# Performance work log

Measured on AMD Instinct MI355X. Metric: run time of the kernel, lower is better.

Reference implementation:

```python
import jax, jax.numpy as jnp
import numpy as np

N_NODES = 50000
N_EDGES = 600000
D = 128
N_LAYERS = 4  # 2 base + 2 resnet layers
N_GRAPHS = 64
NEG_SLOPE = 0.01  # F.leaky_relu default


def setup_inputs() -> dict:
    key = jax.random.key(0)
    k1, k2, k3, k4, k5 = jax.random.split(key, 5)
    x = jax.random.normal(k1, (N_NODES, D), dtype=jnp.float32)
    edge_index = jax.random.randint(k2, (2, N_EDGES), 0, N_NODES, dtype=jnp.int64)
    batch = jnp.sort(jax.random.randint(k3, (N_NODES,), 0, N_GRAPHS, dtype=jnp.int64))
    Wl = jax.random.normal(k4, (N_LAYERS, D, D), dtype=jnp.float32) * 0.05
    bl = jnp.zeros((N_LAYERS, D), dtype=jnp.float32)
    Wr = jax.random.normal(k5, (N_LAYERS, D, D), dtype=jnp.float32) * 0.05
    return {"x": x, "edge_index": edge_index, "batch": batch,
            "Wl": Wl, "bl": bl, "Wr": Wr}


def _mean_aggregate(x, src, dst, n_nodes):
    # mean over incoming neighbors; isolated nodes get 0 (PyG scatter-mean semantics)
    s = jax.ops.segment_sum(x[src], dst, num_segments=n_nodes)  # [N, D]
    cnt = jax.ops.segment_sum(jnp.ones((src.shape[0],), x.dtype), dst,
                              num_segments=n_nodes)
    return s / jnp.maximum(cnt, 1.0)[:, None]


def reference(x, edge_index, batch, Wl, bl, Wr):
    src, dst = edge_index[0], edge_index[1]
    n = x.shape[0]
    for i in range(N_LAYERS):
        agg = _mean_aggregate(x, src, dst, n)                      # [N, D]
        # SAGEConv: lin_l(agg) + lin_r(x); lin_l has bias, lin_r does not
        x_new = agg @ Wl[i].T + bl[i] + x @ Wr[i].T
        x_new = jnp.where(x_new >= 0, x_new, NEG_SLOPE * x_new)    # leaky_relu
        x = x_new if i < 2 else x + x_new                          # residual after first 2
    # global mean pool per graph
    pooled = jax.ops.segment_sum(x, batch, num_segments=N_GRAPHS)  # [G, D]
    counts = jax.ops.segment_sum(jnp.ones((n,), x.dtype), batch,
                                 num_segments=N_GRAPHS)
    return pooled / jnp.maximum(counts, 1.0)[:, None]
```

## Files before the change

kernel.cpp:

```cpp
#include <hip/hip_runtime.h>

#define N_NODES 50000
#define N_EDGES 600000
#define DIM 128
#define N_LAYERS 4
#define N_GRAPHS 64
#define NEG_SLOPE 0.01f
#define NB_SCAN ((N_NODES + 255) / 256)
#define RS 264

typedef __attribute__((ext_vector_type(8))) short short8;
typedef __attribute__((ext_vector_type(16))) float floatx16;

__device__ __forceinline__ unsigned short f2bf(float f) {
    union { float f; unsigned u; } c; c.f = f;
    unsigned u = c.u;
    unsigned r = (u + 0x7FFFu + ((u >> 16) & 1u)) >> 16;
    return (unsigned short)r;
}
__device__ __forceinline__ float bfraw2f(unsigned short b) {
    union { unsigned u; float f; } c; c.u = ((unsigned)b) << 16;
    return c.f;
}
__device__ __forceinline__ float bflo(unsigned u) {
    union { unsigned u; float f; } c; c.u = u << 16; return c.f;
}
__device__ __forceinline__ float bfhi(unsigned u) {
    union { unsigned u; float f; } c; c.u = u & 0xFFFF0000u; return c.f;
}


__global__ void zero_ints(int* p, int n) {
    int i = blockIdx.x * blockDim.x + threadIdx.x;
    if (i < n) p[i] = 0;
}

__global__ void convert_x(const float4* __restrict__ x, uint4* __restrict__ xb) {
    int i = blockIdx.x * blockDim.x + threadIdx.x;
    if (i >= N_NODES * DIM / 8) return;
    float4 a = x[i * 2], b = x[i * 2 + 1];
    uint4 o;
    o.x = ((unsigned)f2bf(a.y) << 16) | f2bf(a.x);
    o.y = ((unsigned)f2bf(a.w) << 16) | f2bf(a.z);
    o.z = ((unsigned)f2bf(b.y) << 16) | f2bf(b.x);
    o.w = ((unsigned)f2bf(b.w) << 16) | f2bf(b.z);
    xb[i] = o;
}

__global__ void pack_w(const float* __restrict__ Wl, const float* __restrict__ Wr,
                       ushort* __restrict__ wpk) {
    int s = blockIdx.x >> 2, t = blockIdx.x & 3;
    int m = blockIdx.y, layer = blockIdx.z;
    int l = threadIdx.x;
    const float* W = ((m == 0) ? Wl : Wr) + (size_t)layer * DIM * DIM;
    int n = t * 32 + (l & 31);
    int kb = s * 16 + (l >> 5) * 8;
    size_t off = ((((size_t)(layer * 2 + m) * 8 + s) * 4 + t) * 64 + l) * 8;
    for (int j = 0; j < 8; j++)
        wpk[off + j] = f2bf(W[n * DIM + kb + j]);
}

__global__ void count_deg(const int* __restrict__ dst, int* deg) {
    int e = blockIdx.x * blockDim.x + threadIdx.x;
    if (e < N_EDGES) atomicAdd(&deg[dst[e]], 1);
}

__global__ void scan_pass1(const int* __restrict__ deg, int* __restrict__ bsum) {
    int i = blockIdx.x * 256 + threadIdx.x;
    int v = (i < N_NODES) ? deg[i] : 0;
    for (int off = 32; off > 0; off >>= 1) v += __shfl_down(v, off, 64);
    __shared__ int ws[4];
    int lane = threadIdx.x & 63, w = threadIdx.x >> 6;
    if (lane == 0) ws[w] = v;
    __syncthreads();
    if (threadIdx.x == 0) bsum[blockIdx.x] = ws[0] + ws[1] + ws[2] + ws[3];
}

__global__ void scan_pass2(int* __restrict__ bsum) {
    __shared__ int sm[256];
    int t = threadIdx.x;
    int v = (t < NB_SCAN) ? bsum[t] : 0;
    sm[t] = v;
    __syncthreads();
    for (int off = 1; off < 256; off <<= 1) {
        int u = (t >= off) ? sm[t - off] : 0;
        __syncthreads();
        sm[t] += u;
        __syncthreads();
    }
    if (t < NB_SCAN) bsum[t] = sm[t] - v;
}

__global__ void scan_pass3(const int* __restrict__ deg, const int* __restrict__ bsum,
                           int* __restrict__ rp) {
    int i = blockIdx.x * 256 + threadIdx.x;
    int v = (i < N_NODES) ? deg[i] : 0;
    int lane = threadIdx.x & 63, w = threadIdx.x >> 6;
    int s = v;
    for (int off = 1; off < 64; off <<= 1) {
        int t = __shfl_up(s, off, 64);
        if (lane >= off) s += t;
    }
    __shared__ int ws[4];
    if (lane == 63) ws[w] = s;
    __syncthreads();
    int wo = 0;
    for (int k = 0; k < 4; k++) wo += (k < w) ? ws[k] : 0;
    int incl = s + wo + bsum[blockIdx.x];
    if (i < N_NODES) rp[i + 1] = incl;
    if (i == 0) rp[0] = 0;
}

__global__ void fill_csr(const int* __restrict__ src, const int* __restrict__ dst,
                         const int* __restrict__ rp, int* __restrict__ fill,
                         int* __restrict__ csr) {
    int e = blockIdx.x * blockDim.x + threadIdx.x;
    if (e >= N_EDGES) return;
    int d = dst[e];
    int pos = atomicAdd(&fill[d], 1);
    csr[rp[d] + pos] = src[e];
}

__global__ void graph_start(const int* __restrict__ batch, int* __restrict__ gstart) {
    int i = blockIdx.x * blockDim.x + threadIdx.x;
    if (i >= N_NODES) return;
    int b = batch[i];
    if (i == 0) {
        for (int g = 0; g <= b; g++) gstart[g] = 0;
    } else {
        int p = batch[i - 1];
        for (int g = p + 1; g <= b; g++) gstart[g] = i;
    }
    if (i == N_NODES - 1) {
        for (int g = b + 1; g <= N_GRAPHS; g++) gstart[g] = N_NODES;
    }
}

__global__ __launch_bounds__(256) void agg_mean_bf16(const uint4* __restrict__ xb4,
                                                     const int* __restrict__ rp,
                                                     const int* __restrict__ csr,
                                                     uint4* __restrict__ agg4) {
    int node = blockIdx.x * 16 + (threadIdx.x >> 4);
    int ln = threadIdx.x & 15;
    if (node >= N_NODES) return;
    int s = rp[node], e = rp[node + 1];
    float a0 = 0.f, a1 = 0.f, a2 = 0.f, a3 = 0.f, a4 = 0.f, a5 = 0.f, a6 = 0.f, a7 = 0.f;
    int i = s;
    for (; i + 2 <= e; i += 2) {
        int n0 = csr[i], n1 = csr[i + 1];
        uint4 v0 = xb4[n0 * 16 + ln];
        uint4 v1 = xb4[n1 * 16 + ln];
        a0 += bflo(v0.x) + bflo(v1.x); a1 += bfhi(v0.x) + bfhi(v1.x);
        a2 += bflo(v0.y) + bflo(v1.y); a3 += bfhi(v0.y) + bfhi(v1.y);
        a4 += bflo(v0.z) + bflo(v1.z); a5 += bfhi(v0.z) + bfhi(v1.z);
        a6 += bflo(v0.w) + bflo(v1.w); a7 += bfhi(v0.w) + bfhi(v1.w);
    }
    if (i < e) {
        uint4 v = xb4[csr[i] * 16 + ln];
        a0 += bflo(v.x); a1 += bfhi(v.x);
        a2 += bflo(v.y); a3 += bfhi(v.y);
        a4 += bflo(v.z); a5 += bfhi(v.z);
        a6 += bflo(v.w); a7 += bfhi(v.w);
    }
    float inv = 1.0f / (float)max(e - s, 1);
    uint4 o;
    o.x = ((unsigned)f2bf(a1 * inv) << 16) | f2bf(a0 * inv);
    o.y = ((unsigned)f2bf(a3 * inv) << 16) | f2bf(a2 * inv);
    o.z = ((unsigned)f2bf(a5 * inv) << 16) | f2bf(a4 * inv);
    o.w = ((unsigned)f2bf(a7 * inv) << 16) | f2bf(a6 * inv);
    agg4[node * 16 + ln] = o;
}

__global__ __launch_bounds__(256) void fused_layer_mfma(const ushort* __restrict__ agg,
                                                        const ushort* __restrict__ xin,
                                                        ushort* __restrict__ xout,
                                                        const ushort* __restrict__ wpk,
                                                        const float* __restrict__ bias,
                                                        int residual) {
    __shared__ ushort sA[128 * RS];
    int t = threadIdx.x;
    int node0 = blockIdx.x * 128;

    const uint4* aggv = (const uint4*)(agg + (size_t)node0 * DIM);
    const uint4* xv   = (const uint4*)(xin + (size_t)node0 * DIM);
    for (int i = t; i < 128 * 32; i += 256) {
        int r = i >> 5, c = i & 31;
        uint4 val = make_uint4(0u, 0u, 0u, 0u);
        if (node0 + r < N_NODES)
            val = (c < 16) ? aggv[r * 16 + c] : xv[r * 16 + (c - 16)];
        *(uint4*)&sA[r * RS + c * 8] = val;
    }
    __syncthreads();

    int wv = t >> 6, l = t & 63;
    int m0 = wv * 32;
    const ushort* arow = &sA[(m0 + (l & 31)) * RS];
    int khalf = (l >> 5) * 8;

    floatx16 acc0, acc1, acc2, acc3;
    for (int ii = 0; ii < 16; ii++) acc0[ii] = acc1[ii] = acc2[ii] = acc3[ii] = 0.f;

    const ushort* wl8 = wpk + (size_t)l * 8;
#pragma unroll
    for (int s2 = 0; s2 < 16; s2++) {
        int m = s2 >> 3, s = s2 & 7;
        short8 a = *(const short8*)(arow + m * 128 + s * 16 + khalf);
        size_t fb = (size_t)((m * 8 + s) * 4) * 512;
        short8 b0 = *(const short8*)(wl8 + fb);
        short8 b1 = *(const short8*)(wl8 + fb + 512);
        short8 b2 = *(const short8*)(wl8 + fb + 1024);
        short8 b3 = *(const short8*)(wl8 + fb + 1536);
        acc0 = __builtin_amdgcn_mfma_f32_32x32x16_bf16(a, b0, acc0, 0, 0, 0);
        acc1 = __builtin_amdgcn_mfma_f32_32x32x16_bf16(a, b1, acc1, 0, 0, 0);
        acc2 = __builtin_amdgcn_mfma_f32_32x32x16_bf16(a, b2, acc2, 0, 0, 0);
        acc3 = __builtin_amdgcn_mfma_f32_32x32x16_bf16(a, b3, acc3, 0, 0, 0);
    }

    int col = l & 31;
    int rbase = 4 * (l >> 5);
    floatx16 accs[4] = {acc0, acc1, acc2, acc3};
    for (int t4 = 0; t4 < 4; t4++) {
        int n = t4 * 32 + col;
        float bv = bias[n];
#pragma unroll
        for (int r = 0; r < 16; r++) {
            int row = (r & 3) + 8 * (r >> 2) + rbase;
            int gm = m0 + row;
            int gn = node0 + gm;
            if (gn >= N_NODES) continue;
            float v = accs[t4][r] + bv;
            v = (v >= 0.f) ? v : NEG_SLOPE * v;
            if (residual) v += bfraw2f(sA[gm * RS + 128 + n]);
            xout[(size_t)gn * DIM + n] = f2bf(v);
        }
    }
}

__global__ __launch_bounds__(128) void pool_partial(const ushort* __restrict__ xb,
                                                    const int* __restrict__ batch,
                                                    float* __restrict__ pooled) {
    int nb = blockIdx.x * 128;
    int ne = min(nb + 128, N_NODES);
    int d = threadIdx.x;
    int gcur = batch[nb];
    float acc = 0.f;
    for (int n = nb; n < ne; n++) {
        int g = batch[n];
        if (g != gcur) {
            atomicAdd(&pooled[gcur * DIM + d], acc);
            acc = 0.f;
            gcur = g;
        }
        acc += bfraw2f(xb[(size_t)n * DIM + d]);
    }
    atomicAdd(&pooled[gcur * DIM + d], acc);
}

__global__ void pool_final(const float* __restrict__ pooled,
                           const int* __restrict__ gstart,
                           float* __restrict__ out) {
    int i = blockIdx.x * blockDim.x + threadIdx.x;
    if (i >= N_GRAPHS * DIM) return;
    int g = i >> 7;
    int cnt = gstart[g + 1] - gstart[g];
    out[i] = pooled[i] / (float)max(cnt, 1);
}


extern "C" void kernel_launch(void* const* d_in, const int* in_sizes, int n_in,
                              void* d_out, int out_size, void* d_ws, size_t ws_size,
                              hipStream_t stream) {
    const float* x     = (const float*)d_in[0];
    const int*   ei    = (const int*)d_in[1];
    const int*   batch = (const int*)d_in[2];
    const float* Wl    = (const float*)d_in[3];
    const float* bl    = (const float*)d_in[4];
    const float* Wr    = (const float*)d_in[5];
    float* out = (float*)d_out;

    const int* esrc = ei;
    const int* edst = ei + N_EDGES;

    ushort* xb0  = (ushort*)d_ws;
    ushort* xbuf = xb0 + (size_t)N_NODES * DIM;
    ushort* agg  = xbuf + (size_t)N_NODES * DIM;
    ushort* wpk  = agg + (size_t)N_NODES * DIM;
    int* deg    = (int*)(wpk + (size_t)N_LAYERS * 2 * DIM * DIM);
    int* fill   = deg + N_NODES;
    int* csr    = fill + N_NODES;
    int* rp     = csr + N_EDGES;
    int* gstart = rp + (N_NODES + 1);
    int* bsum   = gstart + (N_GRAPHS + 1);
    float* pooled = (float*)(bsum + NB_SCAN);

    zero_ints<<<(2 * N_NODES + 255) / 256, 256, 0, stream>>>(deg, 2 * N_NODES);
    zero_ints<<<(N_GRAPHS * DIM + 255) / 256, 256, 0, stream>>>((int*)pooled, N_GRAPHS * DIM);

    convert_x<<<(N_NODES * DIM / 8 + 255) / 256, 256, 0, stream>>>((const float4*)x, (uint4*)xb0);
    pack_w<<<dim3(32, 2, 4), 64, 0, stream>>>(Wl, Wr, wpk);
    count_deg<<<(N_EDGES + 255) / 256, 256, 0, stream>>>(edst, deg);

    scan_pass1<<<NB_SCAN, 256, 0, stream>>>(deg, bsum);
    scan_pass2<<<1, 256, 0, stream>>>(bsum);
    scan_pass3<<<NB_SCAN, 256, 0, stream>>>(deg, bsum, rp);

    fill_csr<<<(N_EDGES + 255) / 256, 256, 0, stream>>>(esrc, edst, rp, fill, csr);
    graph_start<<<(N_NODES + 255) / 256, 256, 0, stream>>>(batch, gstart);

    int agg_blocks = (N_NODES + 15) / 16;
    int gemm_blocks = (N_NODES + 127) / 128;
    for (int l = 0; l < N_LAYERS; l++) {
        const ushort* xin = (l == 0) ? xb0 : xbuf;
        agg_mean_bf16<<<agg_blocks, 256, 0, stream>>>((const uint4*)xin, rp, csr, (uint4*)agg);
        fused_layer_mfma<<<gemm_blocks, 256, 0, stream>>>(
            agg, xin, xbuf, wpk + (size_t)l * 2 * DIM * DIM,
            bl + (size_t)l * DIM, (l >= 2) ? 1 : 0);
    }

    pool_partial<<<(N_NODES + 127) / 128, 128, 0, stream>>>(xbuf, batch, pooled);
    pool_final<<<(N_GRAPHS * DIM + 255) / 256, 256, 0, stream>>>(pooled, gstart, out);
}
```

Measured before the change: 378.5 us.

## Aggregate neighbors with one wavefront per node and shuffle-broadcast CSR indices

```diff
diff --git a/kernel.cpp b/kernel.cpp
--- a/kernel.cpp
+++ b/kernel.cpp
@@ -136,39 +136,33 @@
     }
 }
 
-__global__ __launch_bounds__(256) void agg_mean_bf16(const uint4* __restrict__ xb4,
+__global__ __launch_bounds__(256) void agg_mean_wave(const uint* __restrict__ x32,
                                                      const int* __restrict__ rp,
                                                      const int* __restrict__ csr,
-                                                     uint4* __restrict__ agg4) {
-    int node = blockIdx.x * 16 + (threadIdx.x >> 4);
-    int ln = threadIdx.x & 15;
+                                                     uint* __restrict__ agg32) {
+    int wv = threadIdx.x >> 6, lane = threadIdx.x & 63;
+    int node = blockIdx.x * 4 + wv;
     if (node >= N_NODES) return;
     int s = rp[node], e = rp[node + 1];
-    float a0 = 0.f, a1 = 0.f, a2 = 0.f, a3 = 0.f, a4 = 0.f, a5 = 0.f, a6 = 0.f, a7 = 0.f;
-    int i = s;
-    for (; i + 2 <= e; i += 2) {
-        int n0 = csr[i], n1 = csr[i + 1];
-        uint4 v0 = xb4[n0 * 16 + ln];
-        uint4 v1 = xb4[n1 * 16 + ln];
-        a0 += bflo(v0.x) + bflo(v1.x); a1 += bfhi(v0.x) + bfhi(v1.x);
-        a2 += bflo(v0.y) + bflo(v1.y); a3 += bfhi(v0.y) + bfhi(v1.y);
-        a4 += bflo(v0.z) + bflo(v1.z); a5 += bfhi(v0.z) + bfhi(v1.z);
-        a6 += bflo(v0.w) + bflo(v1.w); a7 += bfhi(v0.w) + bfhi(v1.w);
-    }
-    if (i < e) {
-        uint4 v = xb4[csr[i] * 16 + ln];
-        a0 += bflo(v.x); a1 += bfhi(v.x);
-        a2 += bflo(v.y); a3 += bfhi(v.y);
-        a4 += bflo(v.z); a5 += bfhi(v.z);
-        a6 += bflo(v.w); a7 += bfhi(v.w);
+    float a0 = 0.f, a1 = 0.f;
+    for (int base = s; base < e; base += 64) {
+        int cnt = min(64, e - base);
+        unsigned myidx = (base + lane < e) ? (unsigned)csr[base + lane] : 0u;
+        for (int j = 0; j < cnt; j += 8) {
+            int c2 = min(8, cnt - j);
+            unsigned v[8];
+#pragma unroll
+            for (int k = 0; k < 8; k++) {
+                unsigned idx = __shfl(myidx, j + k, 64);
+                v[k] = (k < c2) ? x32[(size_t)idx * 64 + lane] : 0u;
+            }
+#pragma unroll
+            for (int k = 0; k < 8; k++) { a0 += bflo(v[k]); a1 += bfhi(v[k]); }
+        }
     }
     float inv = 1.0f / (float)max(e - s, 1);
-    uint4 o;
-    o.x = ((unsigned)f2bf(a1 * inv) << 16) | f2bf(a0 * inv);
-    o.y = ((unsigned)f2bf(a3 * inv) << 16) | f2bf(a2 * inv);
-    o.z = ((unsigned)f2bf(a5 * inv) << 16) | f2bf(a4 * inv);
-    o.w = ((unsigned)f2bf(a7 * inv) << 16) | f2bf(a6 * inv);
-    agg4[node * 16 + ln] = o;
+    unsigned o = ((unsigned)f2bf(a1 * inv) << 16) | f2bf(a0 * inv);
+    agg32[(size_t)node * 64 + lane] = o;
 }
 
 __global__ __launch_bounds__(256) void fused_layer_mfma(const ushort* __restrict__ agg,
@@ -307,11 +301,11 @@
     fill_csr<<<(N_EDGES + 255) / 256, 256, 0, stream>>>(esrc, edst, rp, fill, csr);
     graph_start<<<(N_NODES + 255) / 256, 256, 0, stream>>>(batch, gstart);
 
-    int agg_blocks = (N_NODES + 15) / 16;
+    int agg_blocks = (N_NODES + 3) / 4;
     int gemm_blocks = (N_NODES + 127) / 128;
     for (int l = 0; l < N_LAYERS; l++) {
         const ushort* xin = (l == 0) ? xb0 : xbuf;
-        agg_mean_bf16<<<agg_blocks, 256, 0, stream>>>((const uint4*)xin, rp, csr, (uint4*)agg);
+        agg_mean_wave<<<agg_blocks, 256, 0, stream>>>((const uint*)xin, rp, csr, (uint*)agg);
         fused_layer_mfma<<<gemm_blocks, 256, 0, stream>>>(
             agg, xin, xbuf, wpk + (size_t)l * 2 * DIM * DIM,
             bl + (size_t)l * DIM, (l >= 2) ? 1 : 0);
```

After: 375.0 us. About the same (-0.9%).

## Parallelize neighbor aggregation across edges with wave-wide shuffle reduction and feature slicing

Applied to the files above, without the earlier changes.

```diff
diff --git a/kernel.cpp b/kernel.cpp
--- a/kernel.cpp
+++ b/kernel.cpp
@@ -136,39 +136,45 @@
     }
 }
 
-__global__ __launch_bounds__(256) void agg_mean_bf16(const uint4* __restrict__ xb4,
-                                                     const int* __restrict__ rp,
-                                                     const int* __restrict__ csr,
-                                                     uint4* __restrict__ agg4) {
-    int node = blockIdx.x * 16 + (threadIdx.x >> 4);
-    int ln = threadIdx.x & 15;
+__global__ __launch_bounds__(256) void agg_pass(const uint4* __restrict__ x16B,
+                                                const int* __restrict__ rp,
+                                                const int* __restrict__ csr,
+                                                uint4* __restrict__ agg16B) {
+    int wv = threadIdx.x >> 6, lane = threadIdx.x & 63;
+    int node = blockIdx.x * 4 + wv;
+    int p = blockIdx.y;
     if (node >= N_NODES) return;
     int s = rp[node], e = rp[node + 1];
+    int e16 = lane >> 2, q = lane & 3;
     float a0 = 0.f, a1 = 0.f, a2 = 0.f, a3 = 0.f, a4 = 0.f, a5 = 0.f, a6 = 0.f, a7 = 0.f;
-    int i = s;
-    for (; i + 2 <= e; i += 2) {
-        int n0 = csr[i], n1 = csr[i + 1];
-        uint4 v0 = xb4[n0 * 16 + ln];
-        uint4 v1 = xb4[n1 * 16 + ln];
-        a0 += bflo(v0.x) + bflo(v1.x); a1 += bfhi(v0.x) + bfhi(v1.x);
-        a2 += bflo(v0.y) + bflo(v1.y); a3 += bfhi(v0.y) + bfhi(v1.y);
-        a4 += bflo(v0.z) + bflo(v1.z); a5 += bfhi(v0.z) + bfhi(v1.z);
-        a6 += bflo(v0.w) + bflo(v1.w); a7 += bfhi(v0.w) + bfhi(v1.w);
-    }
-    if (i < e) {
-        uint4 v = xb4[csr[i] * 16 + ln];
+    for (int base = s; base < e; base += 16) {
+        int ei = base + e16;
+        uint4 v = make_uint4(0u, 0u, 0u, 0u);
+        if (ei < e) {
+            unsigned idx = (unsigned)csr[ei];
+            v = x16B[(size_t)idx * 16 + p * 4 + q];
+        }
         a0 += bflo(v.x); a1 += bfhi(v.x);
         a2 += bflo(v.y); a3 += bfhi(v.y);
         a4 += bflo(v.z); a5 += bfhi(v.z);
         a6 += bflo(v.w); a7 += bfhi(v.w);
     }
-    float inv = 1.0f / (float)max(e - s, 1);
-    uint4 o;
-    o.x = ((unsigned)f2bf(a1 * inv) << 16) | f2bf(a0 * inv);
-    o.y = ((unsigned)f2bf(a3 * inv) << 16) | f2bf(a2 * inv);
-    o.z = ((unsigned)f2bf(a5 * inv) << 16) | f2bf(a4 * inv);
-    o.w = ((unsigned)f2bf(a7 * inv) << 16) | f2bf(a6 * inv);
-    agg4[node * 16 + ln] = o;
+#pragma unroll
+    for (int off = 4; off < 64; off <<= 1) {
+        a0 += __shfl_xor(a0, off, 64); a1 += __shfl_xor(a1, off, 64);
+        a2 += __shfl_xor(a2, off, 64); a3 += __shfl_xor(a3, off, 64);
+        a4 += __shfl_xor(a4, off, 64); a5 += __shfl_xor(a5, off, 64);
+        a6 += __shfl_xor(a6, off, 64); a7 += __shfl_xor(a7, off, 64);
+    }
+    if (e16 == 0) {
+        float inv = 1.0f / (float)max(e - s, 1);
+        uint4 o;
+        o.x = ((unsigned)f2bf(a1 * inv) << 16) | f2bf(a0 * inv);
+        o.y = ((unsigned)f2bf(a3 * inv) << 16) | f2bf(a2 * inv);
+        o.z = ((unsigned)f2bf(a5 * inv) << 16) | f2bf(a4 * inv);
+        o.w = ((unsigned)f2bf(a7 * inv) << 16) | f2bf(a6 * inv);
+        agg16B[(size_t)node * 16 + p * 4 + q] = o;
+    }
 }
 
 __global__ __launch_bounds__(256) void fused_layer_mfma(const ushort* __restrict__ agg,
@@ -307,11 +313,11 @@
     fill_csr<<<(N_EDGES + 255) / 256, 256, 0, stream>>>(esrc, edst, rp, fill, csr);
     graph_start<<<(N_NODES + 255) / 256, 256, 0, stream>>>(batch, gstart);
 
-    int agg_blocks = (N_NODES + 15) / 16;
+    int aggx = (N_NODES + 3) / 4;
     int gemm_blocks = (N_NODES + 127) / 128;
     for (int l = 0; l < N_LAYERS; l++) {
         const ushort* xin = (l == 0) ? xb0 : xbuf;
-        agg_mean_bf16<<<agg_blocks, 256, 0, stream>>>((const uint4*)xin, rp, csr, (uint4*)agg);
+        agg_pass<<<dim3(aggx, 4), 256, 0, stream>>>((const uint4*)xin, rp, csr, (uint4*)agg);
         fused_layer_mfma<<<gemm_blocks, 256, 0, stream>>>(
             agg, xin, xbuf, wpk + (size_t)l * 2 * DIM * DIM,
             bl + (size_t)l * DIM, (l >= 2) ? 1 : 0);
```

Result: slower. 552.5 us (+46.0%).
